# Performance work log

Hardware: AMD Instinct MI355X
Metric: run time of the kernel (lower is better)

Reference implementation:

```python
import jax, jax.numpy as jnp
import numpy as np

# SS2D config: d_model=96, ssm_ratio=2 -> d_inner=192, d_state=16, dt_rank=ceil(96/16)=6, K=4
B_, H_, W_, DM = 4, 32, 32, 96
DI = 2 * DM          # d_inner = 192
N_STATE = 16
R_DT = 6
K = 4


def setup_inputs() -> dict:
    key = jax.random.key(0)
    ks = jax.random.split(key, 8)
    sc = lambda k, shape, s: jax.random.normal(k, shape, jnp.float32) * s
    A_logs = jnp.log(jnp.tile(jnp.arange(1, N_STATE + 1, dtype=jnp.float32)[None, :], (K * DI, 1)))
    return {
        "x": jax.random.normal(ks[0], (B_, H_, W_, DM), jnp.float32),
        "in_proj_w": sc(ks[1], (2 * DI, DM), 0.05),
        "conv_w": sc(ks[2], (DI, 1, 3, 3), 0.1),      # depthwise 3x3
        "conv_b": jnp.zeros((DI,), jnp.float32),
        "x_proj_weight": sc(ks[3], (K, R_DT + 2 * N_STATE, DI), 0.05),
        "dt_projs_weight": sc(ks[4], (K, DI, R_DT), 0.1),
        "dt_projs_bias": sc(ks[5], (K, DI), 0.1),
        "A_logs": A_logs,
        "Ds": jnp.ones((K * DI,), jnp.float32),
        "ln_gamma": jnp.ones((DI,), jnp.float32),
        "ln_beta": jnp.zeros((DI,), jnp.float32),
        "out_proj_w": sc(ks[6], (DM, DI), 0.05),
    }


def _selective_scan(xs, dts, As, Bs, Cs, Ds, delta_bias):
    # xs, dts: (B,K,D,L); As: (K,D,N); Bs, Cs: (B,K,N,L); Ds, delta_bias: (K,D)
    delta = jax.nn.softplus(dts + delta_bias[None, :, :, None])          # (B,K,D,L)
    dA = jnp.exp(jnp.einsum('bkdl,kdn->lbkdn', delta, As))               # (L,B,K,D,N)
    dBu = jnp.einsum('bkdl,bknl->lbkdn', delta * xs, Bs)                 # (L,B,K,D,N)

    def step(h, inp):
        dA_t, dBu_t = inp
        h = dA_t * h + dBu_t
        return h, h

    h0 = jnp.zeros(dA.shape[1:], dA.dtype)
    _, hs = jax.lax.scan(step, h0, (dA, dBu))                            # (L,B,K,D,N)
    ys = jnp.einsum('lbkdn,bknl->bkdl', hs, Cs)
    return ys + Ds[None, :, :, None] * xs


def reference(x, in_proj_w, conv_w, conv_b, x_proj_weight, dt_projs_weight,
              dt_projs_bias, A_logs, Ds, ln_gamma, ln_beta, out_proj_w):
    B, H, W, _ = x.shape
    L = H * W
    Rr = dt_projs_weight.shape[2]
    Nn = (x_proj_weight.shape[1] - Rr) // 2

    # in_proj -> split into ssm input and gate z
    xz = x @ in_proj_w.T                                                 # (B,H,W,2*DI)
    xi, z = jnp.split(xz, 2, axis=-1)

    # depthwise conv + SiLU
    xc = jnp.transpose(xi, (0, 3, 1, 2))                                 # (B,DI,H,W)
    Dch = xc.shape[1]
    xc = jax.lax.conv_general_dilated(
        xc, conv_w, window_strides=(1, 1), padding='SAME',
        feature_group_count=Dch,
        dimension_numbers=('NCHW', 'OIHW', 'NCHW')) + conv_b[None, :, None, None]
    xc = jax.nn.silu(xc)

    # 4-directional serialization: HW, WH, and their reverses
    x_flat = xc.reshape(B, Dch, L)
    x_t = jnp.transpose(xc, (0, 1, 3, 2)).reshape(B, Dch, L)
    x_hwwh = jnp.stack([x_flat, x_t], axis=1)                            # (B,2,D,L)
    xs = jnp.concatenate([x_hwwh, jnp.flip(x_hwwh, axis=-1)], axis=1)    # (B,4,D,L)

    x_dbl = jnp.einsum('bkdl,kcd->bkcl', xs, x_proj_weight)
    dts, Bs, Cs = jnp.split(x_dbl, [Rr, Rr + Nn], axis=2)
    dts = jnp.einsum('bkrl,kdr->bkdl', dts, dt_projs_weight)

    As = -jnp.exp(A_logs).reshape(4, Dch, Nn)
    Ds_ = Ds.reshape(4, Dch)
    out_y = _selective_scan(xs, dts, As, Bs, Cs, Ds_, dt_projs_bias)     # (B,4,D,L)

    inv_y = jnp.flip(out_y[:, 2:4], axis=-1)
    wh = lambda t: jnp.transpose(t.reshape(B, Dch, W, H), (0, 1, 3, 2)).reshape(B, Dch, L)
    y = out_y[:, 0] + inv_y[:, 0] + wh(out_y[:, 1]) + wh(inv_y[:, 1])
    y = jnp.transpose(y, (0, 2, 1)).reshape(B, H, W, Dch)

    # LayerNorm over channels
    mu = y.mean(-1, keepdims=True)
    var = ((y - mu) ** 2).mean(-1, keepdims=True)
    y = (y - mu) / jnp.sqrt(var + 1e-5) * ln_gamma + ln_beta

    y = y * jax.nn.silu(z)
    return y @ out_proj_w.T
```

## Files before the change

kernel.cpp:

```cpp
#include <hip/hip_runtime.h>
#include <hip/hip_bf16.h>
#include <hip/hip_fp16.h>

#define B_  4
#define H_  32
#define W_  32
#define DM  96
#define DI  192
#define NST 16
#define RDT 6
#define KD  4
#define L_  1024
#define C38 38

#define OFF_WT    0
#define OFF_XPW4  36864
#define OFF_OPW4  66048
#define OFF_DTW   90624
#define OFF_DTB   95232
#define OFF_ALOG  96000
#define OFF_DS    108288
#define OFF_GAM   109056
#define OFF_BET   109248
#define NCANON    109440

typedef __hip_bfloat16 bf16;

__device__ __forceinline__ float b2f(bf16 v) { return __bfloat162float(v); }
__device__ __forceinline__ float san(float v) { return fminf(fmaxf(v, -1.0e4f), 1.0e4f); }
__device__ __forceinline__ float ld_in(const void* p, int i, bool f32) {
    return f32 ? ((const float*)p)[i] : b2f(((const bf16*)p)[i]);
}

union H8 { float4 f4; __half2 h2[4]; };
__device__ __forceinline__ float h8get(const H8& v, int j) {
    return (j & 1) ? __high2float(v.h2[j >> 1]) : __low2float(v.h2[j >> 1]);
}
__device__ __forceinline__ void h8set(H8& v, int j, float f) {
    __half h = __float2half(f);
    if (j & 1) v.h2[j >> 1] = __halves2half2(__low2half(v.h2[j >> 1]), h);
    else       v.h2[j >> 1] = __halves2half2(h, __high2half(v.h2[j >> 1]));
}

__global__ __launch_bounds__(256) void k_canon(
        const void* inw, const void* xpw, const void* dtw, const void* alog,
        const void* opw, const void* a768, const void* b768,
        const void* a192, const void* b192, const void* c192,
        float* __restrict__ wc) {
    int j = blockIdx.x * 256 + threadIdx.x;
    if (j > NCANON) return;
    unsigned wa = ((const unsigned*)a192)[0];
    unsigned wb = ((const unsigned*)b192)[0];
    bool f32;
    const void *gam, *bet;
    if (wa != 0u)      { gam = a192; bet = c192; f32 = (wa == 0x3F800000u); }
    else if (wb != 0u) { gam = b192; bet = c192; f32 = (wb == 0x3F800000u); }
    else               { gam = c192; bet = b192;
                         f32 = (((const unsigned*)c192)[0] == 0x3F800000u); }
    unsigned ones = f32 ? 0x3F800000u : 0x3F803F80u;
    const void *Ds, *dtb;
    if (((const unsigned*)a768)[0] == ones) { Ds = a768; dtb = b768; }
    else                                    { Ds = b768; dtb = a768; }

    if (j == NCANON) { wc[NCANON] = f32 ? 1.f : 0.f; return; }
    float v;
    if (j < OFF_XPW4) {
        int m = j / (2 * DI), c = j % (2 * DI);
        v = ld_in(inw, c * DM + m, f32);
    } else if (j < OFF_OPW4) {
        int j2 = j - OFF_XPW4;
        int r = j2 & 3, q = j2 >> 2;
        int c = q % C38, e = q / C38;
        int k = e / 48, ch = e - k * 48;
        v = ld_in(xpw, (k * C38 + c) * DI + ch * 4 + r, f32);
    } else if (j < OFF_DTW) {
        int j2 = j - OFF_OPW4;
        int r = j2 & 3, q = j2 >> 2;
        int tq = q & 31, dd = q >> 5;
        v = (r < 3) ? ld_in(opw, (tq * 3 + r) * DI + dd, f32) : 0.f;
    } else if (j < OFF_DTB)  v = ld_in(dtw,  j - OFF_DTW,  f32);
    else if (j < OFF_ALOG)   v = ld_in(dtb,  j - OFF_DTB,  f32);
    else if (j < OFF_DS)     v = ld_in(alog, j - OFF_ALOG, f32);
    else if (j < OFF_GAM)    v = ld_in(Ds,   j - OFF_DS,   f32);
    else if (j < OFF_BET)    v = ld_in(gam,  j - OFF_GAM,  f32);
    else                     v = ld_in(bet,  j - OFF_BET,  f32);
    wc[j] = san(v);
}

__global__ __launch_bounds__(768) void k_inproj(
        const void* __restrict__ x, const float* __restrict__ wc,
        __half* __restrict__ xi, __half* __restrict__ gate) {
    __shared__ float xs[DM][20];
    int blk = blockIdx.x;
    int lt = blk & 63, b = blk >> 6;
    int l0 = lt * 16;
    int t = threadIdx.x;
    bool f32 = wc[NCANON] != 0.f;
    for (int idx = t; idx < 16 * DM; idx += 768) {
        int m = idx % DM, li = idx / DM;
        xs[m][li] = san(ld_in(x, (b * L_ + l0 + li) * DM + m, f32));
    }
    __syncthreads();

    int c   = (t < 2 * DI) ? t : t - 2 * DI;
    int li0 = (t < 2 * DI) ? 0 : 8;
    const float* wt = wc + OFF_WT;
    float acc[8];
    #pragma unroll
    for (int j = 0; j < 8; ++j) acc[j] = 0.f;
    for (int m = 0; m < DM; ++m) {
        float wv = wt[m * (2 * DI) + c];
        float4 a0 = *(const float4*)&xs[m][li0];
        float4 a1 = *(const float4*)&xs[m][li0 + 4];
        acc[0] = fmaf(wv, a0.x, acc[0]);
        acc[1] = fmaf(wv, a0.y, acc[1]);
        acc[2] = fmaf(wv, a0.z, acc[2]);
        acc[3] = fmaf(wv, a0.w, acc[3]);
        acc[4] = fmaf(wv, a1.x, acc[4]);
        acc[5] = fmaf(wv, a1.y, acc[5]);
        acc[6] = fmaf(wv, a1.z, acc[6]);
        acc[7] = fmaf(wv, a1.w, acc[7]);
    }

    if (c < DI) {
        H8 o0;
        #pragma unroll
        for (int j = 0; j < 8; ++j) h8set(o0, j, san(acc[j]));
        *(float4*)(xi + (b * DI + c) * L_ + l0 + li0) = o0.f4;
    } else {
        int cg = c - DI;
        #pragma unroll
        for (int j = 0; j < 8; ++j) {
            float z = san(acc[j]);
            float g = z / (1.f + __expf(-z));
            gate[(b * L_ + l0 + li0 + j) * DI + cg] = __float2half(g);
        }
    }
}

__global__ __launch_bounds__(256) void k_conv(
        const __half* __restrict__ xi, const void* __restrict__ cw,
        const void* a192, const void* b192, const void* c192,
        const float* __restrict__ wc,
        __half* __restrict__ xc, __half* __restrict__ xcT) {
    __shared__ __half xin[L_];
    __shared__ __half xtr[33 * 32];
    int blk = blockIdx.x;
    int d = blk % DI, b = blk / DI;
    int t = threadIdx.x;
    const __half* src = xi + (b * DI + d) * L_;
    ((float2*)xin)[t] = ((const float2*)src)[t];

    bool f32 = wc[NCANON] != 0.f;
    unsigned wa = ((const unsigned*)a192)[0];
    unsigned wb = ((const unsigned*)b192)[0];
    const void* cbp;
    if (wa != 0u)      cbp = b192;
    else if (wb != 0u) cbp = a192;
    else               cbp = a192;
    float wgt[9];
    #pragma unroll
    for (int i = 0; i < 9; ++i) wgt[i] = san(ld_in(cw, d * 9 + i, f32));
    float bias = san(ld_in(cbp, d, f32));
    __syncthreads();

    __half* dstN = xc + (b * DI + d) * L_;
    #pragma unroll
    for (int r = 0; r < 4; ++r) {
        int l = r * 256 + t;
        int h = l >> 5, w = l & 31;
        float acc = bias;
        #pragma unroll
        for (int ky = 0; ky < 3; ++ky) {
            int hh = h + ky - 1;
            if (hh < 0 || hh >= H_) continue;
            #pragma unroll
            for (int kx = 0; kx < 3; ++kx) {
                int ww = w + kx - 1;
                if (ww < 0 || ww >= W_) continue;
                acc += __half2float(xin[hh * 32 + ww]) * wgt[ky * 3 + kx];
            }
        }
        acc = san(acc);
        __half v = __float2half(acc / (1.f + __expf(-acc)));
        dstN[l] = v;
        xtr[w * 33 + h] = v;
    }
    __syncthreads();
    __half* dstT = xcT + (b * DI + d) * L_;
    for (int i = t; i < L_; i += 256)
        dstT[i] = xtr[(i >> 5) * 33 + (i & 31)];
}

__global__ __launch_bounds__(256) void k_proj(
        const __half* __restrict__ xc, const __half* __restrict__ xcT,
        const float* __restrict__ wc, __half* __restrict__ xdbl) {
    __shared__ float xs_t[16][196];
    int blk = blockIdx.x;
    int lt = blk & 63, k = (blk >> 6) & 3, b = blk >> 8;
    int l0 = lt * 16;
    int t = threadIdx.x;
    int bk = b * KD + k;

    const __half* base = ((k & 1) ? xcT : xc) + b * DI * L_;
    for (int i = t; i < 16 * DI; i += 256) {
        int li = i & 15, d = i >> 4;
        int l = l0 + li;
        int src = (k < 2) ? l : (L_ - 1 - l);
        xs_t[li][d] = __half2float(base[d * L_ + src]);
    }
    __syncthreads();

    const float* w4 = wc + OFF_XPW4 + k * (48 * C38 * 4);
    for (int o = t; o < 16 * C38; o += 256) {
        int c = o >> 4, li = o & 15;
        const float4* xr = (const float4*)&xs_t[li][0];
        float acc = 0.f;
        #pragma unroll 4
        for (int ch = 0; ch < 48; ++ch) {
            float4 xv = xr[ch];
            float4 wv = *(const float4*)(w4 + (ch * C38 + c) * 4);
            acc += wv.x * xv.x;
            acc += wv.y * xv.y;
            acc += wv.z * xv.z;
            acc += wv.w * xv.w;
        }
        xdbl[(bk * C38 + c) * L_ + l0 + li] = __float2half(san(acc));
    }
}

__global__ __launch_bounds__(256) void k_scan(
        const __half* __restrict__ xdbl, const __half* __restrict__ xc,
        const __half* __restrict__ xcTg, const float* __restrict__ wc,
        __half* __restrict__ yb) {
    __shared__ __half xcN[L_], xcT[L_];
    __shared__ float  ybuf[KD][33 * 32];
    int blk = blockIdx.x;
    int d = blk % DI, b = blk / DI;
    int t = threadIdx.x;
    ((float2*)xcN)[t] = ((const float2*)(xc   + (b * DI + d) * L_))[t];
    ((float2*)xcT)[t] = ((const float2*)(xcTg + (b * DI + d) * L_))[t];

    int k = t >> 6, lane = t & 63;
    int bk = b * KD + k;
    int kd = k * DI + d;
    int l0 = lane * 16;

    float bias = wc[OFF_DTB + kd];
    float wv[RDT];
    #pragma unroll
    for (int r = 0; r < RDT; ++r) wv[r] = wc[OFF_DTW + kd * RDT + r];
    bool fast = true;
    #pragma unroll
    for (int n = 0; n < NST; ++n) {
        float An = -__expf(fminf(wc[OFF_ALOG + kd * NST + n], 30.f));
        if (fabsf(An + (float)(n + 1)) > 1e-3f * (float)(n + 1)) fast = false;
    }

    const __half* xd = xdbl + bk * C38 * L_;
    __syncthreads();

    float de[16];
    #pragma unroll
    for (int j = 0; j < 16; ++j) de[j] = bias;
    #pragma unroll
    for (int r = 0; r < RDT; ++r) {
        H8 v0, v1;
        v0.f4 = *(const float4*)(xd + r * L_ + l0);
        v1.f4 = *(const float4*)(xd + r * L_ + l0 + 8);
        #pragma unroll
        for (int j = 0; j < 8; ++j) {
            de[j]     += wv[r] * h8get(v0, j);
            de[8 + j] += wv[r] * h8get(v1, j);
        }
    }
    float dlt[16], du[16], e[16];
    #pragma unroll
    for (int j = 0; j < 16; ++j) {
        float dl = (de[j] > 20.f) ? de[j] : __logf(1.f + __expf(de[j]));
        dlt[j] = dl;
        int l = l0 + j;
        float u;
        if      (k == 0) u = __half2float(xcN[l]);
        else if (k == 1) u = __half2float(xcT[l]);
        else if (k == 2) u = __half2float(xcN[L_ - 1 - l]);
        else             u = __half2float(xcT[L_ - 1 - l]);
        du[j] = dl * u;
        e[j]  = __expf(-dl);
    }
    float P = 1.f;
    #pragma unroll
    for (int j = 0; j < 16; ++j) P *= e[j];

    float ecur[16];
    #pragma unroll
    for (int j = 0; j < 16; ++j) ecur[j] = e[j];
    float APn = P;
    float y[16];
    #pragma unroll
    for (int j = 0; j < 16; ++j) y[j] = 0.f;

    for (int n = 0; n < NST; ++n) {
        float A;
        if (fast) {
            A = APn;
        } else {
            float An = -__expf(fminf(wc[OFF_ALOG + kd * NST + n], 30.f));
            A = 1.f;
            #pragma unroll
            for (int j = 0; j < 16; ++j) { ecur[j] = __expf(dlt[j] * An); A *= ecur[j]; }
        }
        H8 bv0, bv1, cv0, cv1;
        bv0.f4 = *(const float4*)(xd + (RDT + n) * L_ + l0);
        bv1.f4 = *(const float4*)(xd + (RDT + n) * L_ + l0 + 8);
        cv0.f4 = *(const float4*)(xd + (RDT + NST + n) * L_ + l0);
        cv1.f4 = *(const float4*)(xd + (RDT + NST + n) * L_ + l0 + 8);
        float dub[16];
        #pragma unroll
        for (int j = 0; j < 8; ++j) {
            dub[j]     = du[j]     * h8get(bv0, j);
            dub[8 + j] = du[8 + j] * h8get(bv1, j);
        }
        float hloc = 0.f;
        #pragma unroll
        for (int j = 0; j < 16; ++j) hloc = fmaf(ecur[j], hloc, dub[j]);
        float aa = A, bb = hloc;
        #pragma unroll
        for (int off = 1; off < 64; off <<= 1) {
            float ap = __shfl_up(aa, off);
            float bp = __shfl_up(bb, off);
            bool ok = lane >= off;
            bb = ok ? fmaf(aa, bp, bb) : bb;
            aa = ok ? aa * ap : aa;
        }
        float carry = __shfl_up(bb, 1);
        if (lane == 0) carry = 0.f;
        float hh = carry;
        #pragma unroll
        for (int j = 0; j < 16; ++j) {
            hh = fmaf(ecur[j], hh, dub[j]);
            float Cn = (j < 8) ? h8get(cv0, j) : h8get(cv1, j - 8);
            y[j] = fmaf(Cn, hh, y[j]);
        }
        if (fast) {
            APn *= P;
            #pragma unroll
            for (int j = 0; j < 16; ++j) ecur[j] *= e[j];
        }
    }
    #pragma unroll
    for (int j = 0; j < 16; ++j) {
        int l = l0 + j;
        int idx = (k < 2) ? l : (L_ - 1 - l);
        ybuf[k][(idx >> 5) * 33 + (idx & 31)] = y[j];
    }
    __syncthreads();
    for (int i = t; i < L_; i += 256) {
        int hn = i >> 5, wn = i & 31;
        float v = ybuf[0][hn * 33 + wn] + ybuf[2][hn * 33 + wn]
                + ybuf[1][wn * 33 + hn] + ybuf[3][wn * 33 + hn];
        yb[(b * DI + d) * L_ + i] = __float2half(san(v));
    }
}

__global__ __launch_bounds__(512) void k_merge(
        const __half* __restrict__ yb, const __half* __restrict__ xc,
        const __half* __restrict__ gate, const float* __restrict__ wc,
        float* __restrict__ out) {
    __shared__ float  yd[DI][17];
    __shared__ __half gt[16][DI + 8];
    __shared__ float  red[2][32][16];
    __shared__ float  yg[DI][17];
    __shared__ float  outt[16][DM + 1];
    int blk = blockIdx.x;
    int lt = blk & 63, b = blk >> 6;
    int l0 = lt * 16;
    int tid = threadIdx.x;
    int li = tid & 15, tq = tid >> 4;

    for (int idx = tid; idx < 16 * DI; idx += 512) {
        int l = idx / DI, c = idx % DI;
        gt[l][c] = gate[(b * L_ + l0 + l) * DI + c];
    }
    for (int idx = tid; idx < DI * 16; idx += 512) {
        int d = idx >> 4, l = idx & 15;
        float sD = wc[OFF_DS + d] + wc[OFF_DS + DI + d]
                 + wc[OFF_DS + 2 * DI + d] + wc[OFF_DS + 3 * DI + d];
        float v = __half2float(yb[(b * DI + d) * L_ + l0 + l])
                + sD * __half2float(xc[(b * DI + d) * L_ + l0 + l]);
        yd[d][l] = san(v);
    }
    __syncthreads();

    float s1 = 0.f, s2 = 0.f;
    #pragma unroll
    for (int j = 0; j < 6; ++j) {
        float v = yd[tq * 6 + j][li];
        s1 += v; s2 += v * v;
    }
    red[0][tq][li] = s1; red[1][tq][li] = s2;
    __syncthreads();
    float t1 = 0.f, t2 = 0.f;
    #pragma unroll
    for (int q = 0; q < 32; ++q) { t1 += red[0][q][li]; t2 += red[1][q][li]; }
    float mu  = t1 / DI;
    float var = t2 / DI - mu * mu;
    float inv = rsqrtf(fmaxf(var, 0.f) + 1e-5f);
    #pragma unroll
    for (int j = 0; j < 6; ++j) {
        int d = tq * 6 + j;
        float yn = (yd[d][li] - mu) * inv * wc[OFF_GAM + d] + wc[OFF_BET + d];
        yg[d][li] = yn * __half2float(gt[li][d]);
    }
    __syncthreads();

    float acc0 = 0.f, acc1 = 0.f, acc2 = 0.f;
    #pragma unroll 4
    for (int dd = 0; dd < DI; ++dd) {
        float yv = yg[dd][li];
        float4 w4 = *(const float4*)(wc + OFF_OPW4 + ((dd << 5) + tq) * 4);
        acc0 = fmaf(w4.x, yv, acc0);
        acc1 = fmaf(w4.y, yv, acc1);
        acc2 = fmaf(w4.z, yv, acc2);
    }
    outt[li][tq * 3 + 0] = san(acc0);
    outt[li][tq * 3 + 1] = san(acc1);
    outt[li][tq * 3 + 2] = san(acc2);
    __syncthreads();
    for (int idx = tid; idx < 16 * DM; idx += 512) {
        int l = idx / DM, tm = idx % DM;
        out[(b * L_ + l0 + l) * DM + tm] = outt[l][tm];
    }
}

extern "C" void kernel_launch(void* const* d_in, const int* in_sizes, int n_in,
                              void* d_out, int out_size, void* d_ws, size_t ws_size,
                              hipStream_t stream) {
    const void *x = 0, *inw = 0, *cw = 0, *xpw = 0, *dtw = 0, *alog = 0, *opw = 0;
    const void *p768[2] = {0, 0}, *p192[3] = {0, 0, 0};
    int n768 = 0, n192 = 0;
    for (int i = 0; i < n_in; ++i) {
        switch (in_sizes[i]) {
            case 393216: x    = d_in[i]; break;
            case 36864:  inw  = d_in[i]; break;
            case 1728:   cw   = d_in[i]; break;
            case 29184:  xpw  = d_in[i]; break;
            case 4608:   dtw  = d_in[i]; break;
            case 12288:  alog = d_in[i]; break;
            case 18432:  opw  = d_in[i]; break;
            case 768:    if (n768 < 2) p768[n768++] = d_in[i]; break;
            case 192:    if (n192 < 3) p192[n192++] = d_in[i]; break;
            default: break;
        }
    }

    float* out = (float*)d_out;

    float*  wcp   = (float*)d_ws;
    __half* bufA  = (__half*)(wcp + 109504);
    __half* xcp   = bufA + B_ * DI * L_;
    __half* xcTp  = xcp  + B_ * DI * L_;
    __half* ybp   = xcTp + B_ * DI * L_;
    __half* gatep = ybp  + B_ * DI * L_;

    k_canon <<<(NCANON + 1 + 255) / 256, 256, 0, stream>>>(
        inw, xpw, dtw, alog, opw,
        p768[0], p768[1], p192[0], p192[1], p192[2], wcp);
    k_inproj<<<B_ * (L_ / 16), 768, 0, stream>>>(x, wcp, bufA, gatep);
    k_conv  <<<B_ * DI, 256, 0, stream>>>(bufA, cw, p192[0], p192[1], p192[2],
                                          wcp, xcp, xcTp);
    k_proj  <<<B_ * KD * (L_ / 16), 256, 0, stream>>>(xcp, xcTp, wcp, bufA);
    k_scan  <<<B_ * DI, 256, 0, stream>>>(bufA, xcp, xcTp, wcp, ybp);
    k_merge <<<B_ * (L_ / 16), 512, 0, stream>>>(ybp, xcp, gatep, wcp, out);
}
```

Baseline: 158.3 us.

## Fuse five pipeline kernels into one persistent kernel with global barriers

Replaces the separate in_proj, conv, x_proj, scan and merge launches with a single persistent kernel of 512 blocks. Stages are separated by an atomic-counter grid barrier whose counter is reset by the canon kernel. Work tiling is adjusted to the 256-thread block: 16 tokens per in_proj block, 32 per x_proj block, 8 per merge block. This removes per-launch overhead and inter-kernel gaps. In exchange it relies on all 512 blocks being co-resident, otherwise the spin barrier deadlocks, and it adds spin-wait and barrier costs.

```diff
diff --git a/kernel.cpp b/kernel.cpp
--- a/kernel.cpp
+++ b/kernel.cpp
@@ -12,6 +12,7 @@
 #define KD  4
 #define L_  1024
 #define C38 38
+#define NBLK 512
 
 #define OFF_WT    0
 #define OFF_XPW4  36864
@@ -23,6 +24,7 @@
 #define OFF_GAM   109056
 #define OFF_BET   109248
 #define NCANON    109440
+#define BAR_OFF   109444
 
 typedef __hip_bfloat16 bf16;
 
@@ -40,6 +42,18 @@
     __half h = __float2half(f);
     if (j & 1) v.h2[j >> 1] = __halves2half2(__low2half(v.h2[j >> 1]), h);
     else       v.h2[j >> 1] = __halves2half2(h, __high2half(v.h2[j >> 1]));
+}
+
+__device__ __forceinline__ void gbar(unsigned* bar, unsigned target) {
+    __syncthreads();
+    if (threadIdx.x == 0) {
+        __threadfence();
+        __hip_atomic_fetch_add(bar, 1u, __ATOMIC_ACQ_REL, __HIP_MEMORY_SCOPE_AGENT);
+        while (__hip_atomic_load(bar, __ATOMIC_ACQUIRE, __HIP_MEMORY_SCOPE_AGENT) < target)
+            __builtin_amdgcn_s_sleep(1);
+        __threadfence();
+    }
+    __syncthreads();
 }
 
 __global__ __launch_bounds__(256) void k_canon(
@@ -62,7 +76,11 @@
     if (((const unsigned*)a768)[0] == ones) { Ds = a768; dtb = b768; }
     else                                    { Ds = b768; dtb = a768; }
 
-    if (j == NCANON) { wc[NCANON] = f32 ? 1.f : 0.f; return; }
+    if (j == NCANON) {
+        wc[NCANON] = f32 ? 1.f : 0.f;
+        ((unsigned*)wc)[BAR_OFF] = 0u;
+        return;
+    }
     float v;
     if (j < OFF_XPW4) {
         int m = j / (2 * DI), c = j % (2 * DI);
@@ -87,349 +105,361 @@
     wc[j] = san(v);
 }
 
-__global__ __launch_bounds__(768) void k_inproj(
-        const void* __restrict__ x, const float* __restrict__ wc,
-        __half* __restrict__ xi, __half* __restrict__ gate) {
-    __shared__ float xs[DM][20];
-    int blk = blockIdx.x;
-    int lt = blk & 63, b = blk >> 6;
-    int l0 = lt * 16;
-    int t = threadIdx.x;
-    bool f32 = wc[NCANON] != 0.f;
-    for (int idx = t; idx < 16 * DM; idx += 768) {
-        int m = idx % DM, li = idx / DM;
-        xs[m][li] = san(ld_in(x, (b * L_ + l0 + li) * DM + m, f32));
-    }
-    __syncthreads();
-
-    int c   = (t < 2 * DI) ? t : t - 2 * DI;
-    int li0 = (t < 2 * DI) ? 0 : 8;
-    const float* wt = wc + OFF_WT;
-    float acc[8];
-    #pragma unroll
-    for (int j = 0; j < 8; ++j) acc[j] = 0.f;
-    for (int m = 0; m < DM; ++m) {
-        float wv = wt[m * (2 * DI) + c];
-        float4 a0 = *(const float4*)&xs[m][li0];
-        float4 a1 = *(const float4*)&xs[m][li0 + 4];
-        acc[0] = fmaf(wv, a0.x, acc[0]);
-        acc[1] = fmaf(wv, a0.y, acc[1]);
-        acc[2] = fmaf(wv, a0.z, acc[2]);
-        acc[3] = fmaf(wv, a0.w, acc[3]);
-        acc[4] = fmaf(wv, a1.x, acc[4]);
-        acc[5] = fmaf(wv, a1.y, acc[5]);
-        acc[6] = fmaf(wv, a1.z, acc[6]);
-        acc[7] = fmaf(wv, a1.w, acc[7]);
-    }
-
-    if (c < DI) {
-        H8 o0;
-        #pragma unroll
-        for (int j = 0; j < 8; ++j) h8set(o0, j, san(acc[j]));
-        *(float4*)(xi + (b * DI + c) * L_ + l0 + li0) = o0.f4;
-    } else {
-        int cg = c - DI;
-        #pragma unroll
-        for (int j = 0; j < 8; ++j) {
-            float z = san(acc[j]);
-            float g = z / (1.f + __expf(-z));
-            gate[(b * L_ + l0 + li0 + j) * DI + cg] = __float2half(g);
+__global__ __launch_bounds__(256, 2) void k_mega(
+        const void* __restrict__ x, const void* __restrict__ cw,
+        const void* __restrict__ a192, const void* __restrict__ b192,
+        const void* __restrict__ c192,
+        float* __restrict__ wc, __half* __restrict__ bufA,
+        __half* __restrict__ xc, __half* __restrict__ xcTg,
+        __half* __restrict__ yb, __half* __restrict__ gate,
+        float* __restrict__ out) {
+    __shared__ __align__(16) char smem[26112];
+    const int bid = blockIdx.x, tid = threadIdx.x;
+    unsigned* bar = (unsigned*)wc + BAR_OFF;
+    const bool f32 = wc[NCANON] != 0.f;
+
+    {
+        float (*xs)[20] = reinterpret_cast<float(*)[20]>(smem);
+        for (int vb = bid; vb < 512; vb += NBLK) {
+            int cg = vb & 1, lt = (vb >> 1) & 63, b = vb >> 7;
+            int l0 = lt * 16;
+            for (int idx = tid; idx < 16 * DM; idx += 256) {
+                int m = idx % DM, li = idx / DM;
+                xs[m][li] = san(ld_in(x, (b * L_ + l0 + li) * DM + m, f32));
+            }
+            __syncthreads();
+            if (tid < DI) {
+                int c = cg * DI + tid;
+                const float* wt = wc + OFF_WT;
+                float acc[16];
+                #pragma unroll
+                for (int j = 0; j < 16; ++j) acc[j] = 0.f;
+                for (int m = 0; m < DM; ++m) {
+                    float wv = wt[m * (2 * DI) + c];
+                    float4 a0 = *(const float4*)&xs[m][0];
+                    float4 a1 = *(const float4*)&xs[m][4];
+                    float4 a2 = *(const float4*)&xs[m][8];
+                    float4 a3 = *(const float4*)&xs[m][12];
+                    acc[0]  = fmaf(wv, a0.x, acc[0]);
+                    acc[1]  = fmaf(wv, a0.y, acc[1]);
+                    acc[2]  = fmaf(wv, a0.z, acc[2]);
+                    acc[3]  = fmaf(wv, a0.w, acc[3]);
+                    acc[4]  = fmaf(wv, a1.x, acc[4]);
+                    acc[5]  = fmaf(wv, a1.y, acc[5]);
+                    acc[6]  = fmaf(wv, a1.z, acc[6]);
+                    acc[7]  = fmaf(wv, a1.w, acc[7]);
+                    acc[8]  = fmaf(wv, a2.x, acc[8]);
+                    acc[9]  = fmaf(wv, a2.y, acc[9]);
+                    acc[10] = fmaf(wv, a2.z, acc[10]);
+                    acc[11] = fmaf(wv, a2.w, acc[11]);
+                    acc[12] = fmaf(wv, a3.x, acc[12]);
+                    acc[13] = fmaf(wv, a3.y, acc[13]);
+                    acc[14] = fmaf(wv, a3.z, acc[14]);
+                    acc[15] = fmaf(wv, a3.w, acc[15]);
+                }
+                if (cg == 0) {
+                    H8 o0, o1;
+                    #pragma unroll
+                    for (int j = 0; j < 8; ++j) {
+                        h8set(o0, j, san(acc[j]));
+                        h8set(o1, j, san(acc[8 + j]));
+                    }
+                    float4* dst = (float4*)(bufA + (b * DI + c) * L_ + l0);
+                    dst[0] = o0.f4;
+                    dst[1] = o1.f4;
+                } else {
+                    #pragma unroll
+                    for (int j = 0; j < 16; ++j) {
+                        float z = san(acc[j]);
+                        float g = z / (1.f + __expf(-z));
+                        gate[(b * L_ + l0 + j) * DI + tid] = __float2half(g);
+                    }
+                }
+            }
+            __syncthreads();
         }
     }
-}
-
-__global__ __launch_bounds__(256) void k_conv(
-        const __half* __restrict__ xi, const void* __restrict__ cw,
-        const void* a192, const void* b192, const void* c192,
-        const float* __restrict__ wc,
-        __half* __restrict__ xc, __half* __restrict__ xcT) {
-    __shared__ __half xin[L_];
-    __shared__ __half xtr[33 * 32];
-    int blk = blockIdx.x;
-    int d = blk % DI, b = blk / DI;
-    int t = threadIdx.x;
-    const __half* src = xi + (b * DI + d) * L_;
-    ((float2*)xin)[t] = ((const float2*)src)[t];
-
-    bool f32 = wc[NCANON] != 0.f;
-    unsigned wa = ((const unsigned*)a192)[0];
-    unsigned wb = ((const unsigned*)b192)[0];
-    const void* cbp;
-    if (wa != 0u)      cbp = b192;
-    else if (wb != 0u) cbp = a192;
-    else               cbp = a192;
-    float wgt[9];
-    #pragma unroll
-    for (int i = 0; i < 9; ++i) wgt[i] = san(ld_in(cw, d * 9 + i, f32));
-    float bias = san(ld_in(cbp, d, f32));
-    __syncthreads();
-
-    __half* dstN = xc + (b * DI + d) * L_;
-    #pragma unroll
-    for (int r = 0; r < 4; ++r) {
-        int l = r * 256 + t;
-        int h = l >> 5, w = l & 31;
-        float acc = bias;
-        #pragma unroll
-        for (int ky = 0; ky < 3; ++ky) {
-            int hh = h + ky - 1;
-            if (hh < 0 || hh >= H_) continue;
-            #pragma unroll
-            for (int kx = 0; kx < 3; ++kx) {
-                int ww = w + kx - 1;
-                if (ww < 0 || ww >= W_) continue;
-                acc += __half2float(xin[hh * 32 + ww]) * wgt[ky * 3 + kx];
-            }
+    gbar(bar, NBLK * 1);
+
+    {
+        __half* xin = (__half*)smem;
+        __half* xtr = (__half*)(smem + 2048);
+        unsigned wa = ((const unsigned*)a192)[0];
+        const void* cbp = (wa != 0u) ? b192 : a192;
+        for (int vb = bid; vb < B_ * DI; vb += NBLK) {
+            int d = vb % DI, b = vb / DI;
+            ((float2*)xin)[tid] = ((const float2*)(bufA + (b * DI + d) * L_))[tid];
+            float wgt[9];
+            #pragma unroll
+            for (int i = 0; i < 9; ++i) wgt[i] = san(ld_in(cw, d * 9 + i, f32));
+            float bias = san(ld_in(cbp, d, f32));
+            __syncthreads();
+
+            __half* dstN = xc + (b * DI + d) * L_;
+            #pragma unroll
+            for (int r = 0; r < 4; ++r) {
+                int l = r * 256 + tid;
+                int h = l >> 5, w = l & 31;
+                float acc = bias;
+                #pragma unroll
+                for (int ky = 0; ky < 3; ++ky) {
+                    int hh = h + ky - 1;
+                    if (hh < 0 || hh >= H_) continue;
+                    #pragma unroll
+                    for (int kx = 0; kx < 3; ++kx) {
+                        int ww = w + kx - 1;
+                        if (ww < 0 || ww >= W_) continue;
+                        acc += __half2float(xin[hh * 32 + ww]) * wgt[ky * 3 + kx];
+                    }
+                }
+                acc = san(acc);
+                __half v = __float2half(acc / (1.f + __expf(-acc)));
+                dstN[l] = v;
+                xtr[w * 33 + h] = v;
+            }
+            __syncthreads();
+            __half* dstT = xcTg + (b * DI + d) * L_;
+            for (int i = tid; i < L_; i += 256)
+                dstT[i] = xtr[(i >> 5) * 33 + (i & 31)];
+            __syncthreads();
         }
-        acc = san(acc);
-        __half v = __float2half(acc / (1.f + __expf(-acc)));
-        dstN[l] = v;
-        xtr[w * 33 + h] = v;
-    }
-    __syncthreads();
-    __half* dstT = xcT + (b * DI + d) * L_;
-    for (int i = t; i < L_; i += 256)
-        dstT[i] = xtr[(i >> 5) * 33 + (i & 31)];
-}
-
-__global__ __launch_bounds__(256) void k_proj(
-        const __half* __restrict__ xc, const __half* __restrict__ xcT,
-        const float* __restrict__ wc, __half* __restrict__ xdbl) {
-    __shared__ float xs_t[16][196];
-    int blk = blockIdx.x;
-    int lt = blk & 63, k = (blk >> 6) & 3, b = blk >> 8;
-    int l0 = lt * 16;
-    int t = threadIdx.x;
-    int bk = b * KD + k;
-
-    const __half* base = ((k & 1) ? xcT : xc) + b * DI * L_;
-    for (int i = t; i < 16 * DI; i += 256) {
-        int li = i & 15, d = i >> 4;
-        int l = l0 + li;
-        int src = (k < 2) ? l : (L_ - 1 - l);
-        xs_t[li][d] = __half2float(base[d * L_ + src]);
-    }
-    __syncthreads();
-
-    const float* w4 = wc + OFF_XPW4 + k * (48 * C38 * 4);
-    for (int o = t; o < 16 * C38; o += 256) {
-        int c = o >> 4, li = o & 15;
-        const float4* xr = (const float4*)&xs_t[li][0];
-        float acc = 0.f;
-        #pragma unroll 4
-        for (int ch = 0; ch < 48; ++ch) {
-            float4 xv = xr[ch];
-            float4 wv = *(const float4*)(w4 + (ch * C38 + c) * 4);
-            acc += wv.x * xv.x;
-            acc += wv.y * xv.y;
-            acc += wv.z * xv.z;
-            acc += wv.w * xv.w;
+    }
+    gbar(bar, NBLK * 2);
+
+    {
+        float (*xs_t)[204] = reinterpret_cast<float(*)[204]>(smem);
+        for (int vb = bid; vb < 512; vb += NBLK) {
+            int lt = vb & 31, k = (vb >> 5) & 3, b = vb >> 7;
+            int l0 = lt * 32, bk = b * KD + k;
+            const __half* base = ((k & 1) ? xcTg : xc) + b * DI * L_;
+            for (int i = tid; i < 32 * DI; i += 256) {
+                int li = i & 31, d = i >> 5;
+                int l = l0 + li;
+                int src = (k < 2) ? l : (L_ - 1 - l);
+                xs_t[li][d] = __half2float(base[d * L_ + src]);
+            }
+            __syncthreads();
+            const float* w4 = wc + OFF_XPW4 + k * (48 * C38 * 4);
+            for (int o = tid; o < 32 * C38; o += 256) {
+                int c = o >> 5, li = o & 31;
+                const float4* xr = (const float4*)&xs_t[li][0];
+                float acc = 0.f;
+                #pragma unroll 4
+                for (int ch = 0; ch < 48; ++ch) {
+                    float4 xv = xr[ch];
+                    float4 wv = *(const float4*)(w4 + (ch * C38 + c) * 4);
+                    acc += wv.x * xv.x;
+                    acc += wv.y * xv.y;
+                    acc += wv.z * xv.z;
+                    acc += wv.w * xv.w;
+                }
+                bufA[(bk * C38 + c) * L_ + l0 + li] = __float2half(san(acc));
+            }
+            __syncthreads();
         }
-        xdbl[(bk * C38 + c) * L_ + l0 + li] = __float2half(san(acc));
-    }
-}
-
-__global__ __launch_bounds__(256) void k_scan(
-        const __half* __restrict__ xdbl, const __half* __restrict__ xc,
-        const __half* __restrict__ xcTg, const float* __restrict__ wc,
-        __half* __restrict__ yb) {
-    __shared__ __half xcN[L_], xcT[L_];
-    __shared__ float  ybuf[KD][33 * 32];
-    int blk = blockIdx.x;
-    int d = blk % DI, b = blk / DI;
-    int t = threadIdx.x;
-    ((float2*)xcN)[t] = ((const float2*)(xc   + (b * DI + d) * L_))[t];
-    ((float2*)xcT)[t] = ((const float2*)(xcTg + (b * DI + d) * L_))[t];
-
-    int k = t >> 6, lane = t & 63;
-    int bk = b * KD + k;
-    int kd = k * DI + d;
-    int l0 = lane * 16;
-
-    float bias = wc[OFF_DTB + kd];
-    float wv[RDT];
-    #pragma unroll
-    for (int r = 0; r < RDT; ++r) wv[r] = wc[OFF_DTW + kd * RDT + r];
-    bool fast = true;
-    #pragma unroll
-    for (int n = 0; n < NST; ++n) {
-        float An = -__expf(fminf(wc[OFF_ALOG + kd * NST + n], 30.f));
-        if (fabsf(An + (float)(n + 1)) > 1e-3f * (float)(n + 1)) fast = false;
-    }
-
-    const __half* xd = xdbl + bk * C38 * L_;
-    __syncthreads();
-
-    float de[16];
-    #pragma unroll
-    for (int j = 0; j < 16; ++j) de[j] = bias;
-    #pragma unroll
-    for (int r = 0; r < RDT; ++r) {
-        H8 v0, v1;
-        v0.f4 = *(const float4*)(xd + r * L_ + l0);
-        v1.f4 = *(const float4*)(xd + r * L_ + l0 + 8);
-        #pragma unroll
-        for (int j = 0; j < 8; ++j) {
-            de[j]     += wv[r] * h8get(v0, j);
-            de[8 + j] += wv[r] * h8get(v1, j);
+    }
+    gbar(bar, NBLK * 3);
+
+    {
+        __half* xcN = (__half*)smem;
+        __half* xcT = (__half*)(smem + 2048);
+        float (*ybuf)[33 * 32] = reinterpret_cast<float(*)[33 * 32]>(smem + 4096);
+        const __half* xdblg = bufA;
+        for (int vb = bid; vb < B_ * DI; vb += NBLK) {
+            int d = vb % DI, b = vb / DI;
+            ((float2*)xcN)[tid] = ((const float2*)(xc   + (b * DI + d) * L_))[tid];
+            ((float2*)xcT)[tid] = ((const float2*)(xcTg + (b * DI + d) * L_))[tid];
+
+            int k = tid >> 6, lane = tid & 63;
+            int bk = b * KD + k;
+            int kd = k * DI + d;
+            int l0 = lane * 16;
+
+            float bias = wc[OFF_DTB + kd];
+            float wv[RDT];
+            #pragma unroll
+            for (int r = 0; r < RDT; ++r) wv[r] = wc[OFF_DTW + kd * RDT + r];
+            bool fast = true;
+            #pragma unroll
+            for (int n = 0; n < NST; ++n) {
+                float An = -__expf(fminf(wc[OFF_ALOG + kd * NST + n], 30.f));
+                if (fabsf(An + (float)(n + 1)) > 1e-3f * (float)(n + 1)) fast = false;
+            }
+
+            const __half* xd = xdblg + bk * C38 * L_;
+            __syncthreads();
+
+            float de[16];
+            #pragma unroll
+            for (int j = 0; j < 16; ++j) de[j] = bias;
+            #pragma unroll
+            for (int r = 0; r < RDT; ++r) {
+                H8 v0, v1;
+                v0.f4 = *(const float4*)(xd + r * L_ + l0);
+                v1.f4 = *(const float4*)(xd + r * L_ + l0 + 8);
+                #pragma unroll
+                for (int j = 0; j < 8; ++j) {
+                    de[j]     += wv[r] * h8get(v0, j);
+                    de[8 + j] += wv[r] * h8get(v1, j);
+                }
+            }
+            float dlt[16], du[16], e[16];
+            #pragma unroll
+            for (int j = 0; j < 16; ++j) {
+                float dl = (de[j] > 20.f) ? de[j] : __logf(1.f + __expf(de[j]));
+                dlt[j] = dl;
+                int l = l0 + j;
+                float u;
+                if      (k == 0) u = __half2float(xcN[l]);
+                else if (k == 1) u = __half2float(xcT[l]);
+                else if (k == 2) u = __half2float(xcN[L_ - 1 - l]);
+                else             u = __half2float(xcT[L_ - 1 - l]);
+                du[j] = dl * u;
+                e[j]  = __expf(-dl);
+            }
+            float P = 1.f;
+            #pragma unroll
+            for (int j = 0; j < 16; ++j) P *= e[j];
+
+            float ecur[16];
+            #pragma unroll
+            for (int j = 0; j < 16; ++j) ecur[j] = e[j];
+            float APn = P;
+            float y[16];
+            #pragma unroll
+            for (int j = 0; j < 16; ++j) y[j] = 0.f;
+
+            for (int n = 0; n < NST; ++n) {
+                float A;
+                if (fast) {
+                    A = APn;
+                } else {
+                    float An = -__expf(fminf(wc[OFF_ALOG + kd * NST + n], 30.f));
+                    A = 1.f;
+                    #pragma unroll
+                    for (int j = 0; j < 16; ++j) { ecur[j] = __expf(dlt[j] * An); A *= ecur[j]; }
+                }
+                H8 bv0, bv1, cv0, cv1;
+                bv0.f4 = *(const float4*)(xd + (RDT + n) * L_ + l0);
+                bv1.f4 = *(const float4*)(xd + (RDT + n) * L_ + l0 + 8);
+                cv0.f4 = *(const float4*)(xd + (RDT + NST + n) * L_ + l0);
+                cv1.f4 = *(const float4*)(xd + (RDT + NST + n) * L_ + l0 + 8);
+                float dub[16];
+                #pragma unroll
+                for (int j = 0; j < 8; ++j) {
+                    dub[j]     = du[j]     * h8get(bv0, j);
+                    dub[8 + j] = du[8 + j] * h8get(bv1, j);
+                }
+                float hloc = 0.f;
+                #pragma unroll
+                for (int j = 0; j < 16; ++j) hloc = fmaf(ecur[j], hloc, dub[j]);
+                float aa = A, bb = hloc;
+                #pragma unroll
+                for (int off = 1; off < 64; off <<= 1) {
+                    float ap = __shfl_up(aa, off);
+                    float bp = __shfl_up(bb, off);
+                    bool ok = lane >= off;
+                    bb = ok ? fmaf(aa, bp, bb) : bb;
+                    aa = ok ? aa * ap : aa;
+                }
+                float carry = __shfl_up(bb, 1);
+                if (lane == 0) carry = 0.f;
+                float hh = carry;
+                #pragma unroll
+                for (int j = 0; j < 16; ++j) {
+                    hh = fmaf(ecur[j], hh, dub[j]);
+                    float Cn = (j < 8) ? h8get(cv0, j) : h8get(cv1, j - 8);
+                    y[j] = fmaf(Cn, hh, y[j]);
+                }
+                if (fast) {
+                    APn *= P;
+                    #pragma unroll
+                    for (int j = 0; j < 16; ++j) ecur[j] *= e[j];
+                }
+            }
+            #pragma unroll
+            for (int j = 0; j < 16; ++j) {
+                int l = l0 + j;
+                int idx = (k < 2) ? l : (L_ - 1 - l);
+                ybuf[k][(idx >> 5) * 33 + (idx & 31)] = y[j];
+            }
+            __syncthreads();
+            for (int i = tid; i < L_; i += 256) {
+                int hn = i >> 5, wn = i & 31;
+                float v = ybuf[0][hn * 33 + wn] + ybuf[2][hn * 33 + wn]
+                        + ybuf[1][wn * 33 + hn] + ybuf[3][wn * 33 + hn];
+                yb[(b * DI + d) * L_ + i] = __float2half(san(v));
+            }
+            __syncthreads();
         }
     }
-    float dlt[16], du[16], e[16];
-    #pragma unroll
-    for (int j = 0; j < 16; ++j) {
-        float dl = (de[j] > 20.f) ? de[j] : __logf(1.f + __expf(de[j]));
-        dlt[j] = dl;
-        int l = l0 + j;
-        float u;
-        if      (k == 0) u = __half2float(xcN[l]);
-        else if (k == 1) u = __half2float(xcT[l]);
-        else if (k == 2) u = __half2float(xcN[L_ - 1 - l]);
-        else             u = __half2float(xcT[L_ - 1 - l]);
-        du[j] = dl * u;
-        e[j]  = __expf(-dl);
-    }
-    float P = 1.f;
-    #pragma unroll
-    for (int j = 0; j < 16; ++j) P *= e[j];
-
-    float ecur[16];
-    #pragma unroll
-    for (int j = 0; j < 16; ++j) ecur[j] = e[j];
-    float APn = P;
-    float y[16];
-    #pragma unroll
-    for (int j = 0; j < 16; ++j) y[j] = 0.f;
-
-    for (int n = 0; n < NST; ++n) {
-        float A;
-        if (fast) {
-            A = APn;
-        } else {
-            float An = -__expf(fminf(wc[OFF_ALOG + kd * NST + n], 30.f));
-            A = 1.f;
-            #pragma unroll
-            for (int j = 0; j < 16; ++j) { ecur[j] = __expf(dlt[j] * An); A *= ecur[j]; }
+    gbar(bar, NBLK * 4);
+
+    {
+        float (*yd)[9]    = reinterpret_cast<float(*)[9]>(smem);
+        __half (*gt)[200] = reinterpret_cast<__half(*)[200]>(smem + 6912);
+        float (*red)[32][8] = reinterpret_cast<float(*)[32][8]>(smem + 10112);
+        float (*outt)[97] = reinterpret_cast<float(*)[97]>(smem + 12160);
+        for (int vb = bid; vb < 512; vb += NBLK) {
+            int lt = vb & 127, b = vb >> 7;
+            int l0 = lt * 8;
+            int li = tid & 7, tq = tid >> 3;
+
+            for (int idx = tid; idx < 8 * DI; idx += 256) {
+                int l = idx / DI, c = idx % DI;
+                gt[l][c] = gate[(b * L_ + l0 + l) * DI + c];
+            }
+            for (int idx = tid; idx < DI * 8; idx += 256) {
+                int d = idx >> 3, l = idx & 7;
+                float sD = wc[OFF_DS + d] + wc[OFF_DS + DI + d]
+                         + wc[OFF_DS + 2 * DI + d] + wc[OFF_DS + 3 * DI + d];
+                float v = __half2float(yb[(b * DI + d) * L_ + l0 + l])
+                        + sD * __half2float(xc[(b * DI + d) * L_ + l0 + l]);
+                yd[d][l] = san(v);
+            }
+            __syncthreads();
+
+            float s1 = 0.f, s2 = 0.f;
+            #pragma unroll
+            for (int j = 0; j < 6; ++j) {
+                float v = yd[tq * 6 + j][li];
+                s1 += v; s2 += v * v;
+            }
+            red[0][tq][li] = s1; red[1][tq][li] = s2;
+            __syncthreads();
+            float t1 = 0.f, t2 = 0.f;
+            #pragma unroll
+            for (int q = 0; q < 32; ++q) { t1 += red[0][q][li]; t2 += red[1][q][li]; }
+            float mu  = t1 / DI;
+            float var = t2 / DI - mu * mu;
+            float inv = rsqrtf(fmaxf(var, 0.f) + 1e-5f);
+            #pragma unroll
+            for (int j = 0; j < 6; ++j) {
+                int d = tq * 6 + j;
+                float yn = (yd[d][li] - mu) * inv * wc[OFF_GAM + d] + wc[OFF_BET + d];
+                yd[d][li] = yn * __half2float(gt[li][d]);
+            }
+            __syncthreads();
+
+            float acc0 = 0.f, acc1 = 0.f, acc2 = 0.f;
+            #pragma unroll 4
+            for (int dd = 0; dd < DI; ++dd) {
+                float yv = yd[dd][li];
+                float4 w4 = *(const float4*)(wc + OFF_OPW4 + ((dd << 5) + tq) * 4);
+                acc0 = fmaf(w4.x, yv, acc0);
+                acc1 = fmaf(w4.y, yv, acc1);
+                acc2 = fmaf(w4.z, yv, acc2);
+            }
+            outt[li][tq * 3 + 0] = san(acc0);
+            outt[li][tq * 3 + 1] = san(acc1);
+            outt[li][tq * 3 + 2] = san(acc2);
+            __syncthreads();
+            for (int idx = tid; idx < 8 * DM; idx += 256) {
+                int l = idx / DM, tm = idx % DM;
+                out[(b * L_ + l0 + l) * DM + tm] = outt[l][tm];
+            }
+            __syncthreads();
         }
-        H8 bv0, bv1, cv0, cv1;
-        bv0.f4 = *(const float4*)(xd + (RDT + n) * L_ + l0);
-        bv1.f4 = *(const float4*)(xd + (RDT + n) * L_ + l0 + 8);
-        cv0.f4 = *(const float4*)(xd + (RDT + NST + n) * L_ + l0);
-        cv1.f4 = *(const float4*)(xd + (RDT + NST + n) * L_ + l0 + 8);
-        float dub[16];
-        #pragma unroll
-        for (int j = 0; j < 8; ++j) {
-            dub[j]     = du[j]     * h8get(bv0, j);
-            dub[8 + j] = du[8 + j] * h8get(bv1, j);
-        }
-        float hloc = 0.f;
-        #pragma unroll
-        for (int j = 0; j < 16; ++j) hloc = fmaf(ecur[j], hloc, dub[j]);
-        float aa = A, bb = hloc;
-        #pragma unroll
-        for (int off = 1; off < 64; off <<= 1) {
-            float ap = __shfl_up(aa, off);
-            float bp = __shfl_up(bb, off);
-            bool ok = lane >= off;
-            bb = ok ? fmaf(aa, bp, bb) : bb;
-            aa = ok ? aa * ap : aa;
-        }
-        float carry = __shfl_up(bb, 1);
-        if (lane == 0) carry = 0.f;
-        float hh = carry;
-        #pragma unroll
-        for (int j = 0; j < 16; ++j) {
-            hh = fmaf(ecur[j], hh, dub[j]);
-            float Cn = (j < 8) ? h8get(cv0, j) : h8get(cv1, j - 8);
-            y[j] = fmaf(Cn, hh, y[j]);
-        }
-        if (fast) {
-            APn *= P;
-            #pragma unroll
-            for (int j = 0; j < 16; ++j) ecur[j] *= e[j];
-        }
-    }
-    #pragma unroll
-    for (int j = 0; j < 16; ++j) {
-        int l = l0 + j;
-        int idx = (k < 2) ? l : (L_ - 1 - l);
-        ybuf[k][(idx >> 5) * 33 + (idx & 31)] = y[j];
-    }
-    __syncthreads();
-    for (int i = t; i < L_; i += 256) {
-        int hn = i >> 5, wn = i & 31;
-        float v = ybuf[0][hn * 33 + wn] + ybuf[2][hn * 33 + wn]
-                + ybuf[1][wn * 33 + hn] + ybuf[3][wn * 33 + hn];
-        yb[(b * DI + d) * L_ + i] = __float2half(san(v));
-    }
-}
-
-__global__ __launch_bounds__(512) void k_merge(
-        const __half* __restrict__ yb, const __half* __restrict__ xc,
-        const __half* __restrict__ gate, const float* __restrict__ wc,
-        float* __restrict__ out) {
-    __shared__ float  yd[DI][17];
-    __shared__ __half gt[16][DI + 8];
-    __shared__ float  red[2][32][16];
-    __shared__ float  yg[DI][17];
-    __shared__ float  outt[16][DM + 1];
-    int blk = blockIdx.x;
-    int lt = blk & 63, b = blk >> 6;
-    int l0 = lt * 16;
-    int tid = threadIdx.x;
-    int li = tid & 15, tq = tid >> 4;
-
-    for (int idx = tid; idx < 16 * DI; idx += 512) {
-        int l = idx / DI, c = idx % DI;
-        gt[l][c] = gate[(b * L_ + l0 + l) * DI + c];
-    }
-    for (int idx = tid; idx < DI * 16; idx += 512) {
-        int d = idx >> 4, l = idx & 15;
-        float sD = wc[OFF_DS + d] + wc[OFF_DS + DI + d]
-                 + wc[OFF_DS + 2 * DI + d] + wc[OFF_DS + 3 * DI + d];
-        float v = __half2float(yb[(b * DI + d) * L_ + l0 + l])
-                + sD * __half2float(xc[(b * DI + d) * L_ + l0 + l]);
-        yd[d][l] = san(v);
-    }
-    __syncthreads();
-
-    float s1 = 0.f, s2 = 0.f;
-    #pragma unroll
-    for (int j = 0; j < 6; ++j) {
-        float v = yd[tq * 6 + j][li];
-        s1 += v; s2 += v * v;
-    }
-    red[0][tq][li] = s1; red[1][tq][li] = s2;
-    __syncthreads();
-    float t1 = 0.f, t2 = 0.f;
-    #pragma unroll
-    for (int q = 0; q < 32; ++q) { t1 += red[0][q][li]; t2 += red[1][q][li]; }
-    float mu  = t1 / DI;
-    float var = t2 / DI - mu * mu;
-    float inv = rsqrtf(fmaxf(var, 0.f) + 1e-5f);
-    #pragma unroll
-    for (int j = 0; j < 6; ++j) {
-        int d = tq * 6 + j;
-        float yn = (yd[d][li] - mu) * inv * wc[OFF_GAM + d] + wc[OFF_BET + d];
-        yg[d][li] = yn * __half2float(gt[li][d]);
-    }
-    __syncthreads();
-
-    float acc0 = 0.f, acc1 = 0.f, acc2 = 0.f;
-    #pragma unroll 4
-    for (int dd = 0; dd < DI; ++dd) {
-        float yv = yg[dd][li];
-        float4 w4 = *(const float4*)(wc + OFF_OPW4 + ((dd << 5) + tq) * 4);
-        acc0 = fmaf(w4.x, yv, acc0);
-        acc1 = fmaf(w4.y, yv, acc1);
-        acc2 = fmaf(w4.z, yv, acc2);
-    }
-    outt[li][tq * 3 + 0] = san(acc0);
-    outt[li][tq * 3 + 1] = san(acc1);
-    outt[li][tq * 3 + 2] = san(acc2);
-    __syncthreads();
-    for (int idx = tid; idx < 16 * DM; idx += 512) {
-        int l = idx / DM, tm = idx % DM;
-        out[(b * L_ + l0 + l) * DM + tm] = outt[l][tm];
     }
 }
 
@@ -457,19 +487,16 @@
     float* out = (float*)d_out;
 
     float*  wcp   = (float*)d_ws;
-    __half* bufA  = (__half*)(wcp + 109504);
+    __half* bufA  = (__half*)(wcp + 109456);
     __half* xcp   = bufA + B_ * DI * L_;
     __half* xcTp  = xcp  + B_ * DI * L_;
     __half* ybp   = xcTp + B_ * DI * L_;
     __half* gatep = ybp  + B_ * DI * L_;
 
-    k_canon <<<(NCANON + 1 + 255) / 256, 256, 0, stream>>>(
+    k_canon<<<(NCANON + 1 + 255) / 256, 256, 0, stream>>>(
         inw, xpw, dtw, alog, opw,
         p768[0], p768[1], p192[0], p192[1], p192[2], wcp);
-    k_inproj<<<B_ * (L_ / 16), 768, 0, stream>>>(x, wcp, bufA, gatep);
-    k_conv  <<<B_ * DI, 256, 0, stream>>>(bufA, cw, p192[0], p192[1], p192[2],
-                                          wcp, xcp, xcTp);
-    k_proj  <<<B_ * KD * (L_ / 16), 256, 0, stream>>>(xcp, xcTp, wcp, bufA);
-    k_scan  <<<B_ * DI, 256, 0, stream>>>(bufA, xcp, xcTp, wcp, ybp);
-    k_merge <<<B_ * (L_ / 16), 512, 0, stream>>>(ybp, xcp, gatep, wcp, out);
-}
+    k_mega<<<NBLK, 256, 0, stream>>>(
+        x, cw, p192[0], p192[1], p192[2],
+        wcp, bufA, xcp, xcTp, ybp, gatep, out);
+}
```

After: 442.4 us. 179% more time.
